# Optimization experiments

Hardware: AMD Instinct MI355X
Metric: run time of the kernel (lower is better)

## Reference

```python
import jax, jax.numpy as jnp
import numpy as np

IN_FEATURES = 512
OUT_FEATURES = 512
B_EXP = 2.0
EPS = 1e-12  # torch F.normalize eps


def setup_inputs() -> dict:
    key = jax.random.key(0)
    kz, kw = jax.random.split(key)
    z = jax.random.normal(kz, (100000, IN_FEATURES), dtype=jnp.float32)
    weight = jax.random.normal(kw, (OUT_FEATURES, IN_FEATURES), dtype=jnp.float32) * (1.0 / np.sqrt(IN_FEATURES))
    return {"z": z, "weight": weight}


def reference(z, weight):
    # lin = z @ W^T : [N, out]
    lin = jnp.einsum('ni,oi->no', z, weight)
    # row-wise L2 normalize (torch F.normalize: x / max(||x||, eps))
    z_norm = z / jnp.maximum(jnp.linalg.norm(z, axis=1, keepdims=True), EPS)
    w_norm = weight / jnp.maximum(jnp.linalg.norm(weight, axis=1, keepdims=True), EPS)
    cos = jnp.einsum('ni,oi->no', z_norm, w_norm)
    scale = jnp.abs(cos) ** (B_EXP - 1.0)
    return lin * scale
```

## Files before the change

kernel.cpp:

```cpp
#include <hip/hip_runtime.h>
#include <hip/hip_bf16.h>
#include <stdint.h>


constexpr int KDIM = 512;
constexpr int NDIM = 512;

typedef __attribute__((ext_vector_type(8))) short bf16x8;
typedef __attribute__((ext_vector_type(4))) float f32x4;
typedef __attribute__((ext_vector_type(4))) uint32_t u32x4;

__device__ __forceinline__ uint32_t pk_bf16(float a, float b) {
  __hip_bfloat162 h = __float22bfloat162_rn(make_float2(a, b));
  union { __hip_bfloat162 h2; uint32_t u; } c;
  c.h2 = h;
  return c.u;
}

__device__ __forceinline__ void gload_lds16(const void* g, void* lds) {
  __builtin_amdgcn_global_load_lds(
      (const __attribute__((address_space(1))) uint32_t*)(uintptr_t)g,
      (__attribute__((address_space(3))) uint32_t*)(uintptr_t)lds,
      16, 0, 0);
}

__global__ __launch_bounds__(128) void prep_w(const float* __restrict__ w,
                                              unsigned short* __restrict__ wb,
                                              float* __restrict__ cninv) {
  const int row = blockIdx.x;
  const int t   = threadIdx.x;
  const float* gp = w + (size_t)row * KDIM + t * 4;
  f32x4 v = *(const f32x4*)gp;
  float s = v.x * v.x + v.y * v.y + v.z * v.z + v.w * v.w;

  uint2 p;
  p.x = pk_bf16(v.x, v.y);
  p.y = pk_bf16(v.z, v.w);
  *(uint2*)(wb + (size_t)row * KDIM + t * 4) = p;

  #pragma unroll
  for (int off = 32; off > 0; off >>= 1) s += __shfl_down(s, off, 64);
  __shared__ float red[2];
  if ((t & 63) == 0) red[t >> 6] = s;
  __syncthreads();
  if (t == 0) cninv[row] = 1.0f / fmaxf(sqrtf(red[0] + red[1]), 1e-12f);
}

__global__ __launch_bounds__(256) void gemm_bcos(const float* __restrict__ z,
                                                 const unsigned short* __restrict__ wb,
                                                 const float* __restrict__ cninv,
                                                 float* __restrict__ out, int M) {
  __shared__ unsigned short As[128 * 64];
  __shared__ unsigned short Bs[128 * 64];
  __shared__ float rowsq[128];
  __shared__ float rinv[128];

  const int t    = threadIdx.x;
  const int nb   = blockIdx.x;
  const int mb   = blockIdx.y;
  const int w    = t >> 6;
  const int lane = t & 63;
  const int lrow = lane & 15;
  const int quad = lane >> 4;
  const int wm   = (w & 1) * 64;
  const int wn   = (w >> 1) * 64;

  if (t < 128) rowsq[t] = 0.0f;

  f32x4 acc[4][4];
  #pragma unroll
  for (int i = 0; i < 4; ++i)
    #pragma unroll
    for (int j = 0; j < 4; ++j) acc[i][j] = (f32x4)0.0f;

  int rr[4];
  size_t gbase[4];
  #pragma unroll
  for (int i = 0; i < 4; ++i) {
    int gidx = t + 256 * i;
    rr[i] = gidx >> 3;
    int g = gidx & 7;
    int grow = mb * 128 + rr[i];
    if (grow >= M) grow = M - 1;
    gbase[i] = (size_t)grow * KDIM + g * 8;
  }

  float sq[4] = {0.f, 0.f, 0.f, 0.f};

  for (int kk = 0; kk < 8; ++kk) {
    const int kbase = kk * 64;
    __syncthreads();

    #pragma unroll
    for (int i = 0; i < 4; ++i) {
      int cidx = t + 256 * i;
      int r = cidx >> 3, c = cidx & 7;
      gload_lds16(wb + ((size_t)(nb * 128 + r) * KDIM + kbase + c * 8), &Bs[cidx * 8]);
    }

    #pragma unroll
    for (int i = 0; i < 4; ++i) {
      const float* gp = z + gbase[i] + kbase;
      f32x4 v0 = *(const f32x4*)gp;
      f32x4 v1 = *(const f32x4*)(gp + 4);
      sq[i] += v0.x * v0.x + v0.y * v0.y + v0.z * v0.z + v0.w * v0.w +
               v1.x * v1.x + v1.y * v1.y + v1.z * v1.z + v1.w * v1.w;
      u32x4 p;
      p.x = pk_bf16(v0.x, v0.y);
      p.y = pk_bf16(v0.z, v0.w);
      p.z = pk_bf16(v1.x, v1.y);
      p.w = pk_bf16(v1.z, v1.w);
      *(u32x4*)&As[(t + 256 * i) * 8] = p;
    }

    __syncthreads();

    #pragma unroll
    for (int ks = 0; ks < 2; ++ks) {
      const int k0 = ks * 32 + quad * 8;
      bf16x8 a[4], b[4];
      #pragma unroll
      for (int x = 0; x < 4; ++x) {
        a[x] = *(const bf16x8*)&As[(wm + x * 16 + lrow) * 64 + k0];
        b[x] = *(const bf16x8*)&Bs[(wn + x * 16 + lrow) * 64 + k0];
      }
      #pragma unroll
      for (int mt = 0; mt < 4; ++mt)
        #pragma unroll
        for (int nt = 0; nt < 4; ++nt)
          acc[mt][nt] = __builtin_amdgcn_mfma_f32_16x16x32_bf16(a[mt], b[nt], acc[mt][nt], 0, 0, 0);
    }
  }

  #pragma unroll
  for (int i = 0; i < 4; ++i) atomicAdd(&rowsq[rr[i]], sq[i]);
  __syncthreads();
  if (t < 128) rinv[t] = 1.0f / fmaxf(sqrtf(rowsq[t]), 1e-12f);
  __syncthreads();

  #pragma unroll
  for (int nt = 0; nt < 4; ++nt) {
    const int colg = nb * 128 + wn + nt * 16 + lrow;
    const float cv = cninv[colg];
    #pragma unroll
    for (int mt = 0; mt < 4; ++mt) {
      const int lrm = wm + mt * 16 + quad * 4;
      #pragma unroll
      for (int i = 0; i < 4; ++i) {
        const int rowg = mb * 128 + lrm + i;
        if (rowg < M) {
          const float v = acc[mt][nt][i];
          out[(size_t)rowg * NDIM + colg] = v * fabsf(v) * rinv[lrm + i] * cv;
        }
      }
    }
  }
}

extern "C" void kernel_launch(void* const* d_in, const int* in_sizes, int n_in,
                              void* d_out, int out_size, void* d_ws, size_t ws_size,
                              hipStream_t stream) {
  const float* z = (const float*)d_in[0];
  const float* w = (const float*)d_in[1];
  float* out = (float*)d_out;
  const int M = in_sizes[0] / KDIM;

  unsigned short* wb = (unsigned short*)d_ws;
  float* cninv = (float*)((char*)d_ws + (size_t)NDIM * KDIM * 2);

  prep_w<<<dim3(NDIM), dim3(128), 0, stream>>>(w, wb, cninv);

  dim3 grid(NDIM / 128, (M + 127) / 128);
  gemm_bcos<<<grid, dim3(256), 0, stream>>>(z, wb, cninv, out, M);
}
```

Before: 489.1 us.

## Swizzle LDS tiles, prefetch z into registers, stage epilogue through LDS

XOR-swizzles the A and B tile layouts in shared memory to cut bank conflicts on the MFMA fragment reads. It also software-prefetches the next z chunk into registers so global loads overlap with compute. The epilogue now stages results through shared memory, which is unioned with the GEMM tiles, so each row is written with coalesced 16-byte stores instead of scattered scalar stores. The register prefetch adds register pressure, and the epilogue adds extra LDS traffic.

New measurement: 584.3 us. 19.5% more time.

```diff
diff --git a/kernel.cpp b/kernel.cpp
--- a/kernel.cpp
+++ b/kernel.cpp
@@ -46,12 +46,17 @@
   if (t == 0) cninv[row] = 1.0f / fmaxf(sqrtf(red[0] + red[1]), 1e-12f);
 }
 
+struct SMemMM { unsigned short As[128 * 64]; unsigned short Bs[128 * 64]; };
+union SMemU {
+  SMemMM mm;
+  float ep[4 * 32 * 68];
+};
+
 __global__ __launch_bounds__(256) void gemm_bcos(const float* __restrict__ z,
                                                  const unsigned short* __restrict__ wb,
                                                  const float* __restrict__ cninv,
                                                  float* __restrict__ out, int M) {
-  __shared__ unsigned short As[128 * 64];
-  __shared__ unsigned short Bs[128 * 64];
+  __shared__ SMemU sm;
   __shared__ float rowsq[128];
   __shared__ float rinv[128];
 
@@ -75,34 +80,43 @@
 
   int rr[4];
   size_t gbase[4];
+  int aoff[4];
+  size_t boff[4];
+  int bdst[4];
   #pragma unroll
   for (int i = 0; i < 4; ++i) {
-    int gidx = t + 256 * i;
-    rr[i] = gidx >> 3;
-    int g = gidx & 7;
-    int grow = mb * 128 + rr[i];
+    const int gidx = t + 256 * i;
+    const int r = gidx >> 3, c = gidx & 7;
+    rr[i] = r;
+    int grow = mb * 128 + r;
     if (grow >= M) grow = M - 1;
-    gbase[i] = (size_t)grow * KDIM + g * 8;
+    gbase[i] = (size_t)grow * KDIM + c * 8;
+    aoff[i]  = (r * 8 + (c ^ (r & 7))) * 8;
+    boff[i]  = (size_t)(nb * 128 + r) * KDIM + (size_t)((c ^ (r & 7)) * 8);
+    bdst[i]  = gidx * 8;
   }
 
   float sq[4] = {0.f, 0.f, 0.f, 0.f};
+
+  f32x4 zr0[4], zr1[4];
+  #pragma unroll
+  for (int i = 0; i < 4; ++i) {
+    const float* gp = z + gbase[i];
+    zr0[i] = *(const f32x4*)gp;
+    zr1[i] = *(const f32x4*)(gp + 4);
+  }
 
   for (int kk = 0; kk < 8; ++kk) {
     const int kbase = kk * 64;
     __syncthreads();
 
     #pragma unroll
+    for (int i = 0; i < 4; ++i)
+      gload_lds16(wb + boff[i] + kbase, &sm.mm.Bs[bdst[i]]);
+
+    #pragma unroll
     for (int i = 0; i < 4; ++i) {
-      int cidx = t + 256 * i;
-      int r = cidx >> 3, c = cidx & 7;
-      gload_lds16(wb + ((size_t)(nb * 128 + r) * KDIM + kbase + c * 8), &Bs[cidx * 8]);
-    }
-
-    #pragma unroll
-    for (int i = 0; i < 4; ++i) {
-      const float* gp = z + gbase[i] + kbase;
-      f32x4 v0 = *(const f32x4*)gp;
-      f32x4 v1 = *(const f32x4*)(gp + 4);
+      const f32x4 v0 = zr0[i], v1 = zr1[i];
       sq[i] += v0.x * v0.x + v0.y * v0.y + v0.z * v0.z + v0.w * v0.w +
                v1.x * v1.x + v1.y * v1.y + v1.z * v1.z + v1.w * v1.w;
       u32x4 p;
@@ -110,19 +124,30 @@
       p.y = pk_bf16(v0.z, v0.w);
       p.z = pk_bf16(v1.x, v1.y);
       p.w = pk_bf16(v1.z, v1.w);
-      *(u32x4*)&As[(t + 256 * i) * 8] = p;
+      *(u32x4*)&sm.mm.As[aoff[i]] = p;
+    }
+
+    if (kk < 7) {
+      #pragma unroll
+      for (int i = 0; i < 4; ++i) {
+        const float* gp = z + gbase[i] + kbase + 64;
+        zr0[i] = *(const f32x4*)gp;
+        zr1[i] = *(const f32x4*)(gp + 4);
+      }
     }
 
     __syncthreads();
 
     #pragma unroll
     for (int ks = 0; ks < 2; ++ks) {
-      const int k0 = ks * 32 + quad * 8;
+      const int cc = ks * 4 + quad;
       bf16x8 a[4], b[4];
       #pragma unroll
       for (int x = 0; x < 4; ++x) {
-        a[x] = *(const bf16x8*)&As[(wm + x * 16 + lrow) * 64 + k0];
-        b[x] = *(const bf16x8*)&Bs[(wn + x * 16 + lrow) * 64 + k0];
+        const int ra = wm + x * 16 + lrow;
+        const int rb = wn + x * 16 + lrow;
+        a[x] = *(const bf16x8*)&sm.mm.As[(ra * 8 + (cc ^ (ra & 7))) * 8];
+        b[x] = *(const bf16x8*)&sm.mm.Bs[(rb * 8 + (cc ^ (rb & 7))) * 8];
       }
       #pragma unroll
       for (int mt = 0; mt < 4; ++mt)
@@ -138,21 +163,35 @@
   if (t < 128) rinv[t] = 1.0f / fmaxf(sqrtf(rowsq[t]), 1e-12f);
   __syncthreads();
 
-  #pragma unroll
-  for (int nt = 0; nt < 4; ++nt) {
-    const int colg = nb * 128 + wn + nt * 16 + lrow;
-    const float cv = cninv[colg];
-    #pragma unroll
-    for (int mt = 0; mt < 4; ++mt) {
-      const int lrm = wm + mt * 16 + quad * 4;
-      #pragma unroll
-      for (int i = 0; i < 4; ++i) {
-        const int rowg = mb * 128 + lrm + i;
-        if (rowg < M) {
+  float cv[4];
+  #pragma unroll
+  for (int nt = 0; nt < 4; ++nt) cv[nt] = cninv[nb * 128 + wn + nt * 16 + lrow];
+
+  float* ep = &sm.ep[w * 32 * 68];
+  #pragma unroll
+  for (int ch = 0; ch < 2; ++ch) {
+    #pragma unroll
+    for (int half = 0; half < 2; ++half) {
+      const int mt = ch * 2 + half;
+      #pragma unroll
+      for (int nt = 0; nt < 4; ++nt) {
+        #pragma unroll
+        for (int i = 0; i < 4; ++i) {
+          const int lr = wm + mt * 16 + quad * 4 + i;
           const float v = acc[mt][nt][i];
-          out[(size_t)rowg * NDIM + colg] = v * fabsf(v) * rinv[lrm + i] * cv;
+          ep[(half * 16 + quad * 4 + i) * 68 + nt * 16 + lrow] =
+              v * fabsf(v) * rinv[lr] * cv[nt];
         }
       }
+    }
+    #pragma unroll
+    for (int p = 0; p < 8; ++p) {
+      const int rl = p * 4 + (lane >> 4);
+      const int c4 = (lane & 15) * 4;
+      const f32x4 v = *(const f32x4*)&ep[rl * 68 + c4];
+      const int grow = mb * 128 + wm + ch * 32 + rl;
+      if (grow < M)
+        *(f32x4*)&out[(size_t)grow * NDIM + nb * 128 + wn + c4] = v;
     }
   }
 }
```
